# Kernel optimization log

Hardware: AMD Instinct MI355X
Metric: run time of the kernel (lower is better)

Reference implementation:

```python
import jax, jax.numpy as jnp
import numpy as np

N_NODES = 100000
N_EDGES = 1250000
N_GRAPHS = 1024
NUM_SHAPES = 16
NUM_COLORS = 16
NUM_CLASSES = 10


def setup_inputs() -> dict:
    key = jax.random.key(0)
    ks = jax.random.split(key, 16)
    x_tokens = jax.random.randint(ks[0], (N_NODES, 2), 0, NUM_SHAPES, dtype=jnp.int64) if jax.config.jax_enable_x64 else jax.random.randint(ks[0], (N_NODES, 2), 0, NUM_SHAPES, dtype=jnp.int32)
    edge_index = jax.random.randint(ks[1], (2, N_EDGES), 0, N_NODES, dtype=jnp.int32)
    batch = jnp.sort(jax.random.randint(ks[2], (N_NODES,), 0, N_GRAPHS, dtype=jnp.int32))
    def glorot(k, shape, fan_in):
        return jax.random.normal(k, shape, jnp.float32) / jnp.sqrt(jnp.float32(fan_in))
    return {
        "x_tokens": x_tokens,
        "edge_index": edge_index,
        "batch": batch,
        "shape_emb": jax.random.normal(ks[3], (NUM_SHAPES, 8), jnp.float32),
        "color_emb": jax.random.normal(ks[4], (NUM_COLORS, 8), jnp.float32),
        "lin_w": glorot(ks[5], (32, 16), 16),
        "lin_b": jnp.zeros((32,), jnp.float32),
        "conv1_wrel": glorot(ks[6], (64, 32), 32),
        "conv1_brel": jnp.zeros((64,), jnp.float32),
        "conv1_wroot": glorot(ks[7], (64, 32), 32),
        "conv2_wrel": glorot(ks[8], (64, 64), 64),
        "conv2_brel": jnp.zeros((64,), jnp.float32),
        "conv2_wroot": glorot(ks[9], (64, 64), 64),
        "cls_w": glorot(ks[10], (NUM_CLASSES, 64), 64),
        "cls_b": jnp.zeros((NUM_CLASSES,), jnp.float32),
    }


def _graph_conv(x, src, dst, w_rel, b_rel, w_root):
    # PyG GraphConv (aggr='add'): out_i = W_rel @ sum_{j->i} x_j + b_rel + W_root @ x_i
    agg = jax.ops.segment_sum(x[src], dst, num_segments=x.shape[0])  # [N, d_in]
    return agg @ w_rel.T + b_rel + x @ w_root.T


def reference(x_tokens, edge_index, batch, shape_emb, color_emb, lin_w, lin_b,
              conv1_wrel, conv1_brel, conv1_wroot,
              conv2_wrel, conv2_brel, conv2_wroot, cls_w, cls_b):
    src, dst = edge_index[0], edge_index[1]
    # embed shape/color tokens and concat -> [N, 16]
    x = jnp.concatenate([shape_emb[x_tokens[:, 0]], color_emb[x_tokens[:, 1]]], axis=1)
    x = jax.nn.relu(x @ lin_w.T + lin_b)                      # [N, 32]
    x = jax.nn.relu(_graph_conv(x, src, dst, conv1_wrel, conv1_brel, conv1_wroot))  # [N, 64]
    x = jax.nn.relu(_graph_conv(x, src, dst, conv2_wrel, conv2_brel, conv2_wroot))  # [N, 64]
    # global mean pool over graphs
    sums = jax.ops.segment_sum(x, batch, num_segments=N_GRAPHS)           # [G, 64]
    counts = jax.ops.segment_sum(jnp.ones((x.shape[0],), x.dtype), batch, num_segments=N_GRAPHS)
    pooled = sums / jnp.maximum(counts, 1.0)[:, None]
    return pooled @ cls_w.T + cls_b                            # [G, num_classes]
```

## Files before the change

kernel.cpp:

```cpp
#include <hip/hip_runtime.h>

#define N_NODES  100000
#define N_EDGES  1250000
#define N_GRAPHS 1024
#define NB       ((N_NODES + 127) >> 7)
#define NB2      (N_NODES / 16)
#define NBLK_F   500
#define EPB      (N_EDGES / NBLK_F)
#define EMB_BLKS ((N_NODES + 255) / 256)
#define CAP      512

typedef __attribute__((ext_vector_type(8))) short short8;
typedef __attribute__((ext_vector_type(4))) float f32x4;
union U16 { uint4 u; short8 s; };

__device__ __forceinline__ float bflo(unsigned int w) { return __uint_as_float(w << 16); }
__device__ __forceinline__ float bfhi(unsigned int w) { return __uint_as_float(w & 0xffff0000u); }
__device__ __forceinline__ unsigned short f2bf(float f) {
  unsigned int u = __float_as_uint(f);
  u = (u + 0x7fffu + ((u >> 16) & 1u)) >> 16;
  return (unsigned short)u;
}
__device__ __forceinline__ unsigned int pack2(float a, float b) {
  return (unsigned int)f2bf(a) | ((unsigned int)f2bf(b) << 16);
}

template <int DIN>
__device__ __forceinline__ void prep_body(int t, const float* __restrict__ wrel,
                                          const float* __restrict__ wroot,
                                          unsigned short* __restrict__ Bf) {
  constexpr int NKC = (2 * DIN) / 32;
  if (t >= NKC * 4 * 64) return;
  int l = t & 63;
  int ct = (t >> 6) & 3;
  int kc = t >> 8;
  int col = ct * 16 + (l & 15);
#pragma unroll
  for (int e = 0; e < 8; ++e) {
    int k = kc * 32 + ((l >> 4) << 3) + e;
    float v = (k < DIN) ? wrel[col * DIN + k] : wroot[col * DIN + (k - DIN)];
    Bf[(size_t)t * 8 + e] = f2bf(v);
  }
}

__global__ void __launch_bounds__(256)
k_front(const int* __restrict__ tok,
        const float* __restrict__ semb, const float* __restrict__ cemb,
        const float* __restrict__ lw, const float* __restrict__ lb,
        unsigned short* __restrict__ x1,
        const float* __restrict__ w1rel, const float* __restrict__ w1root,
        const float* __restrict__ w2rel, const float* __restrict__ w2root,
        unsigned short* __restrict__ Bf1, unsigned short* __restrict__ Bf2,
        const int* __restrict__ dst, int* __restrict__ hist) {
  __shared__ int lh[NB];
  const int t = threadIdx.x;
  const int bid = blockIdx.x;
  if (bid < EMB_BLKS) {
    int i = bid * 256 + t;
    if (i >= N_NODES) return;
    int s = tok[2 * i], c = tok[2 * i + 1];
    float e[16];
#pragma unroll
    for (int k = 0; k < 8; ++k) { e[k] = semb[s * 8 + k]; e[8 + k] = cemb[c * 8 + k]; }
    unsigned int w[16];
#pragma unroll
    for (int o = 0; o < 16; ++o) {
      float a0 = lb[2 * o], a1 = lb[2 * o + 1];
#pragma unroll
      for (int k = 0; k < 16; ++k) {
        a0 = fmaf(e[k], lw[(2 * o) * 16 + k], a0);
        a1 = fmaf(e[k], lw[(2 * o + 1) * 16 + k], a1);
      }
      w[o] = pack2(fmaxf(a0, 0.f), fmaxf(a1, 0.f));
    }
    uint4* d4 = (uint4*)(x1 + (size_t)i * 32);
#pragma unroll
    for (int q = 0; q < 4; ++q)
      d4[q] = make_uint4(w[4 * q], w[4 * q + 1], w[4 * q + 2], w[4 * q + 3]);
  } else if (bid < EMB_BLKS + 6) {
    int pb = bid - EMB_BLKS;
    if (pb < 2) prep_body<32>(pb * 256 + t, w1rel, w1root, Bf1);
    else prep_body<64>((pb - 2) * 256 + t, w2rel, w2root, Bf2);
  } else {
    const int blk = bid - EMB_BLKS - 6;
    for (int i = t; i < NB; i += 256) lh[i] = 0;
    __syncthreads();
    const int start = blk * EPB;
    for (int e = start + t; e < start + EPB; e += 256)
      atomicAdd(&lh[dst[e] >> 7], 1);
    __syncthreads();
    int* hrow = hist + (size_t)blk * NB;
    for (int i = t; i < NB; i += 256)
      hrow[i] = lh[i];
  }
}

__global__ void __launch_bounds__(512)
k_colscan(int* __restrict__ hist, int* __restrict__ btotal) {
  __shared__ int sc[512];
  const int b = blockIdx.x;
  const int t = threadIdx.x;
  int v = (t < NBLK_F) ? hist[(size_t)t * NB + b] : 0;
  sc[t] = v;
  __syncthreads();
  for (int off = 1; off < 512; off <<= 1) {
    int x = (t >= off) ? sc[t - off] : 0;
    __syncthreads();
    sc[t] += x;
    __syncthreads();
  }
  if (t < NBLK_F) hist[(size_t)t * NB + b] = sc[t] - v;
  if (t == 511) btotal[b] = sc[511];
}

__global__ void __launch_bounds__(1024)
k_bscan(const int* __restrict__ btotal, int* __restrict__ bbase) {
  __shared__ int s[1024];
  int t = threadIdx.x;
  int d = (t < NB) ? btotal[t] : 0;
  s[t] = d;
  __syncthreads();
  for (int off = 1; off < 1024; off <<= 1) {
    int v = (t >= off) ? s[t - off] : 0;
    __syncthreads();
    s[t] += v;
    __syncthreads();
  }
  if (t < NB) bbase[t] = s[t] - d;
}

__global__ void __launch_bounds__(256)
k_bfill(const int* __restrict__ src, const int* __restrict__ dst,
        const int* __restrict__ bbase, const int* __restrict__ hist,
        int* __restrict__ tmp) {
  __shared__ int cur[NB];
  const int t = threadIdx.x;
  const int blk = blockIdx.x;
  const int* hrow = hist + (size_t)blk * NB;
  for (int i = t; i < NB; i += 256)
    cur[i] = bbase[i] + hrow[i];
  __syncthreads();
  const int start = blk * EPB;
  for (int e = start + t; e < start + EPB; e += 256) {
    int d = dst[e];
    int pos = atomicAdd(&cur[d >> 7], 1);
    tmp[pos] = (src[e] << 7) | (d & 127);
  }
}

__global__ void __launch_bounds__(256)
k_bfinal(const int* __restrict__ bbase, const int* __restrict__ btotal,
         const int* __restrict__ tmp,
         int* __restrict__ deg, int* __restrict__ rowst,
         int* __restrict__ esrc) {
  __shared__ int h[128], sc[128], cur[128];
  const int t = threadIdx.x;
  const int b = blockIdx.x;
  const int base = bbase[b], cnt = btotal[b];
  if (t < 128) h[t] = 0;
  __syncthreads();
  for (int i = t; i < cnt; i += 256) atomicAdd(&h[tmp[base + i] & 127], 1);
  __syncthreads();
  if (t < 128) sc[t] = h[t];
  __syncthreads();
  for (int off = 1; off < 128; off <<= 1) {
    int v = 0;
    if (t < 128 && t >= off) v = sc[t - off];
    __syncthreads();
    if (t < 128) sc[t] += v;
    __syncthreads();
  }
  if (t < 128) {
    int excl = sc[t] - h[t];
    cur[t] = excl;
    int node = (b << 7) + t;
    if (node < N_NODES) { deg[node] = h[t]; rowst[node] = base + excl; }
  }
  __syncthreads();
  for (int i = t; i < cnt; i += 256) {
    int v = tmp[base + i];
    int p = atomicAdd(&cur[v & 127], 1);
    esrc[base + p] = v >> 7;
  }
}

template <int DIN>
__global__ void __launch_bounds__(256)
k_conv(const int* __restrict__ deg, const int* __restrict__ rowst,
       const int* __restrict__ esrc,
       const unsigned short* __restrict__ X,
       const uint4* __restrict__ Bf,
       const float* __restrict__ bias,
       unsigned short* __restrict__ Y) {
  constexpr int NKC = (2 * DIN) / 32;
  constexpr int LPGu = DIN / 4;
  constexpr int GROUPS = 64 / LPGu;
  __shared__ int lsrc[CAP];
  __shared__ int hdeg[16], hbase[16];
  __shared__ int s_cnt, s_base;
  __shared__ unsigned short aggT[(DIN / 8) * 16 * 8];
  const int t = threadIdx.x;
  const int lane = t & 63;
  const int wv = t >> 6;
  const int b = blockIdx.x;
  if (t < 16) hdeg[t] = deg[b * 16 + t];
  __syncthreads();
  if (t == 0) {
    int run = 0;
#pragma unroll
    for (int n = 0; n < 16; ++n) { hbase[n] = run; run += hdeg[n]; }
    s_cnt = min(run, CAP);
    s_base = rowst[b * 16];
  }
  __syncthreads();
  const int cnt = s_cnt, base = s_base;
  for (int i = t; i < cnt; i += 256) lsrc[i] = esrc[base + i];
  __syncthreads();

  const int sub = lane / LPGu;
  const int lg = lane % LPGu;
#pragma unroll
  for (int k = 0; k < 4; ++k) {
    const int n = wv * 4 + k;
    const int dgn = hdeg[n];
    const int eb = hbase[n];
    float a0 = 0.f, a1 = 0.f, a2 = 0.f, a3 = 0.f;
    for (int j = 0; j < dgn; j += 2 * GROUPS) {
      int e0 = j + sub, e1 = j + GROUPS + sub;
      int s0 = lsrc[min(eb + min(e0, dgn - 1), CAP - 1)];
      int s1 = lsrc[min(eb + min(e1, dgn - 1), CAP - 1)];
      uint2 r0 = *((const uint2*)(X + (size_t)s0 * DIN) + lg);
      uint2 r1 = *((const uint2*)(X + (size_t)s1 * DIN) + lg);
      if (e0 < dgn) { a0 += bflo(r0.x); a1 += bfhi(r0.x); a2 += bflo(r0.y); a3 += bfhi(r0.y); }
      if (e1 < dgn) { a0 += bflo(r1.x); a1 += bfhi(r1.x); a2 += bflo(r1.y); a3 += bfhi(r1.y); }
    }
#pragma unroll
    for (int off = LPGu; off < 64; off <<= 1) {
      a0 += __shfl_xor(a0, off);
      a1 += __shfl_xor(a1, off);
      a2 += __shfl_xor(a2, off);
      a3 += __shfl_xor(a3, off);
    }
    if (sub == 0) {
      uint2 w; w.x = pack2(a0, a1); w.y = pack2(a2, a3);
      *(uint2*)&aggT[(((lg >> 1) * 16 + n) << 3) + ((lg & 1) << 2)] = w;
    }
  }
  __syncthreads();

  short8 bf[NKC];
#pragma unroll
  for (int kc = 0; kc < NKC; ++kc) { U16 u; u.u = Bf[(kc * 4 + wv) * 64 + lane]; bf[kc] = u.s; }
  const float bc = bias[wv * 16 + (lane & 15)];
  const int r = lane & 15;
  const int gg = b * 16 + r;
  short8 a[NKC];
#pragma unroll
  for (int kc = 0; kc < NKC / 2; ++kc) {
    const int chunk = kc * 4 + (lane >> 4);
    U16 u; u.u = *(const uint4*)&aggT[(chunk * 16 + r) << 3];
    a[kc] = u.s;
  }
#pragma unroll
  for (int kc = NKC / 2; kc < NKC; ++kc) {
    const int colx = (kc - NKC / 2) * 32 + ((lane >> 4) << 3);
    U16 u; u.u = *(const uint4*)(X + (size_t)gg * DIN + colx);
    a[kc] = u.s;
  }
  f32x4 acc = {bc, bc, bc, bc};
#pragma unroll
  for (int kc = 0; kc < NKC; ++kc)
    acc = __builtin_amdgcn_mfma_f32_16x16x32_bf16(a[kc], bf[kc], acc, 0, 0, 0);
  const int col = wv * 16 + (lane & 15);
#pragma unroll
  for (int j = 0; j < 4; ++j) {
    int grow = b * 16 + ((lane >> 4) << 2) + j;
    Y[(size_t)grow * 64 + col] = f2bf(fmaxf(acc[j], 0.f));
  }
}

__global__ void __launch_bounds__(256)
k_pool(const unsigned short* __restrict__ y2,
       const int* __restrict__ batch,
       const float* __restrict__ cw, const float* __restrict__ cb,
       float* __restrict__ out) {
  __shared__ float part[4][64];
  const int g = blockIdx.x;
  const int lane = threadIdx.x & 63;
  const int wv = threadIdx.x >> 6;
  int lo = 0, hi = N_NODES;
  while (lo < hi) { int m = (lo + hi) >> 1; if (batch[m] < g) lo = m + 1; else hi = m; }
  int lo2 = lo, hi2 = N_NODES;
  while (lo2 < hi2) { int m = (lo2 + hi2) >> 1; if (batch[m] < g + 1) lo2 = m + 1; else hi2 = m; }
  float s = 0.f;
  for (int r = lo + wv; r < lo2; r += 4)
    s += __uint_as_float((unsigned int)y2[(size_t)r * 64 + lane] << 16);
  part[wv][lane] = s;
  __syncthreads();
  if (wv == 0) {
    float p = part[0][lane] + part[1][lane] + part[2][lane] + part[3][lane];
    int c_ = lo2 - lo;
    p *= 1.f / (float)(c_ > 0 ? c_ : 1);
    for (int c = 0; c < 10; ++c) {
      float v = p * cw[c * 64 + lane];
#pragma unroll
      for (int off = 1; off < 64; off <<= 1) v += __shfl_xor(v, off);
      if (lane == 0) out[g * 10 + c] = v + cb[c];
    }
  }
}

extern "C" void kernel_launch(void* const* d_in, const int* in_sizes, int n_in,
                              void* d_out, int out_size, void* d_ws, size_t ws_size,
                              hipStream_t stream) {
  const int*   tok    = (const int*)d_in[0];
  const int*   eidx   = (const int*)d_in[1];
  const int*   batch  = (const int*)d_in[2];
  const float* semb   = (const float*)d_in[3];
  const float* cemb   = (const float*)d_in[4];
  const float* lw     = (const float*)d_in[5];
  const float* lb     = (const float*)d_in[6];
  const float* w1rel  = (const float*)d_in[7];
  const float* b1     = (const float*)d_in[8];
  const float* w1root = (const float*)d_in[9];
  const float* w2rel  = (const float*)d_in[10];
  const float* b2     = (const float*)d_in[11];
  const float* w2root = (const float*)d_in[12];
  const float* cw     = (const float*)d_in[13];
  const float* cb     = (const float*)d_in[14];
  const int* src = eidx;
  const int* dst = eidx + N_EDGES;

  char* p = (char*)d_ws;
  unsigned short* X1 = (unsigned short*)p;  p += (size_t)N_NODES * 32 * 2;
  unsigned short* X2 = (unsigned short*)p;  p += (size_t)N_NODES * 64 * 2;
  unsigned short* Y2 = (unsigned short*)p;  p += (size_t)N_NODES * 64 * 2;
  int*   tmp    = (int*)p;  p += (size_t)N_EDGES * 4;
  int*   esrc   = (int*)p;  p += (size_t)N_EDGES * 4;
  int*   degv   = (int*)p;  p += (size_t)N_NODES * 4;
  int*   rowst  = (int*)p;  p += (size_t)N_NODES * 4;
  int*   hist   = (int*)p;  p += (size_t)NBLK_F * NB * 4;
  int*   btotal = (int*)p;  p += 4096;
  int*   bbase  = (int*)p;  p += 4096;
  unsigned short* Bf1 = (unsigned short*)p;  p += 512 * 8 * 2;
  unsigned short* Bf2 = (unsigned short*)p;  p += 1024 * 8 * 2;

  k_front<<<EMB_BLKS + 6 + NBLK_F, 256, 0, stream>>>(
      tok, semb, cemb, lw, lb, X1,
      w1rel, w1root, w2rel, w2root, Bf1, Bf2, dst, hist);

  k_colscan<<<NB, 512, 0, stream>>>(hist, btotal);
  k_bscan<<<1, 1024, 0, stream>>>(btotal, bbase);
  k_bfill<<<NBLK_F, 256, 0, stream>>>(src, dst, bbase, hist, tmp);
  k_bfinal<<<NB, 256, 0, stream>>>(bbase, btotal, tmp, degv, rowst, esrc);

  k_conv<32><<<NB2, 256, 0, stream>>>(degv, rowst, esrc, X1, (const uint4*)Bf1, b1, X2);
  k_conv<64><<<NB2, 256, 0, stream>>>(degv, rowst, esrc, X2, (const uint4*)Bf2, b2, Y2);

  k_pool<<<N_GRAPHS, 256, 0, stream>>>(Y2, batch, cw, cb, (float*)d_out);
}
```

Measured before the change: 135.4 us.

## Fold bucket-base scan into fill/final kernels and widen conv gathers to 16B

Drops the single-block k_bscan launch. Each k_bfill block now recomputes the exclusive scan of btotal redundantly, and each k_bfinal block computes its base by reducing the preceding btotal entries, which removes one launch and its serialization gap. The conv aggregation also switches from 8-byte to 16-byte row loads per lane, so fewer lanes cover each row and more edges are processed in parallel per wave. The cost is redundant scan work in every block and more accumulator registers.

New measurement: 151.9 us. +12.1%, slower.

```diff
diff --git a/kernel.cpp b/kernel.cpp
--- a/kernel.cpp
+++ b/kernel.cpp
@@ -113,32 +113,37 @@
   if (t == 511) btotal[b] = sc[511];
 }
 
-__global__ void __launch_bounds__(1024)
-k_bscan(const int* __restrict__ btotal, int* __restrict__ bbase) {
-  __shared__ int s[1024];
-  int t = threadIdx.x;
-  int d = (t < NB) ? btotal[t] : 0;
-  s[t] = d;
-  __syncthreads();
-  for (int off = 1; off < 1024; off <<= 1) {
-    int v = (t >= off) ? s[t - off] : 0;
-    __syncthreads();
-    s[t] += v;
-    __syncthreads();
-  }
-  if (t < NB) bbase[t] = s[t] - d;
-}
-
 __global__ void __launch_bounds__(256)
 k_bfill(const int* __restrict__ src, const int* __restrict__ dst,
-        const int* __restrict__ bbase, const int* __restrict__ hist,
+        const int* __restrict__ btotal, const int* __restrict__ hist,
         int* __restrict__ tmp) {
   __shared__ int cur[NB];
+  __shared__ int spart[256];
   const int t = threadIdx.x;
   const int blk = blockIdx.x;
   const int* hrow = hist + (size_t)blk * NB;
-  for (int i = t; i < NB; i += 256)
-    cur[i] = bbase[i] + hrow[i];
+  int v[4]; int s = 0;
+#pragma unroll
+  for (int j = 0; j < 4; ++j) {
+    int idx = t * 4 + j;
+    v[j] = (idx < NB) ? btotal[idx] : 0;
+    s += v[j];
+  }
+  spart[t] = s;
+  __syncthreads();
+  for (int off = 1; off < 256; off <<= 1) {
+    int x = (t >= off) ? spart[t - off] : 0;
+    __syncthreads();
+    spart[t] += x;
+    __syncthreads();
+  }
+  int run = spart[t] - s;
+#pragma unroll
+  for (int j = 0; j < 4; ++j) {
+    int idx = t * 4 + j;
+    if (idx < NB) cur[idx] = run + hrow[idx];
+    run += v[j];
+  }
   __syncthreads();
   const int start = blk * EPB;
   for (int e = start + t; e < start + EPB; e += 256) {
@@ -149,16 +154,26 @@
 }
 
 __global__ void __launch_bounds__(256)
-k_bfinal(const int* __restrict__ bbase, const int* __restrict__ btotal,
-         const int* __restrict__ tmp,
+k_bfinal(const int* __restrict__ btotal, const int* __restrict__ tmp,
          int* __restrict__ deg, int* __restrict__ rowst,
          int* __restrict__ esrc) {
+  __shared__ int spart[256];
   __shared__ int h[128], sc[128], cur[128];
+  __shared__ int s_base;
   const int t = threadIdx.x;
   const int b = blockIdx.x;
-  const int base = bbase[b], cnt = btotal[b];
+  int s = 0;
+  for (int i = t; i < b; i += 256) s += btotal[i];
+  spart[t] = s;
   if (t < 128) h[t] = 0;
   __syncthreads();
+  for (int off = 128; off >= 1; off >>= 1) {
+    if (t < off) spart[t] += spart[t + off];
+    __syncthreads();
+  }
+  if (t == 0) s_base = spart[0];
+  __syncthreads();
+  const int base = s_base, cnt = btotal[b];
   for (int i = t; i < cnt; i += 256) atomicAdd(&h[tmp[base + i] & 127], 1);
   __syncthreads();
   if (t < 128) sc[t] = h[t];
@@ -193,8 +208,8 @@
        const float* __restrict__ bias,
        unsigned short* __restrict__ Y) {
   constexpr int NKC = (2 * DIN) / 32;
-  constexpr int LPGu = DIN / 4;
-  constexpr int GROUPS = 64 / LPGu;
+  constexpr int LPG = DIN / 8;
+  constexpr int GROUPS = 64 / LPG;
   __shared__ int lsrc[CAP];
   __shared__ int hdeg[16], hbase[16];
   __shared__ int s_cnt, s_base;
@@ -217,33 +232,42 @@
   for (int i = t; i < cnt; i += 256) lsrc[i] = esrc[base + i];
   __syncthreads();
 
-  const int sub = lane / LPGu;
-  const int lg = lane % LPGu;
+  const int sub = lane / LPG;
+  const int lg = lane % LPG;
 #pragma unroll
   for (int k = 0; k < 4; ++k) {
     const int n = wv * 4 + k;
     const int dgn = hdeg[n];
     const int eb = hbase[n];
     float a0 = 0.f, a1 = 0.f, a2 = 0.f, a3 = 0.f;
+    float a4 = 0.f, a5 = 0.f, a6 = 0.f, a7 = 0.f;
     for (int j = 0; j < dgn; j += 2 * GROUPS) {
       int e0 = j + sub, e1 = j + GROUPS + sub;
       int s0 = lsrc[min(eb + min(e0, dgn - 1), CAP - 1)];
       int s1 = lsrc[min(eb + min(e1, dgn - 1), CAP - 1)];
-      uint2 r0 = *((const uint2*)(X + (size_t)s0 * DIN) + lg);
-      uint2 r1 = *((const uint2*)(X + (size_t)s1 * DIN) + lg);
-      if (e0 < dgn) { a0 += bflo(r0.x); a1 += bfhi(r0.x); a2 += bflo(r0.y); a3 += bfhi(r0.y); }
-      if (e1 < dgn) { a0 += bflo(r1.x); a1 += bfhi(r1.x); a2 += bflo(r1.y); a3 += bfhi(r1.y); }
-    }
-#pragma unroll
-    for (int off = LPGu; off < 64; off <<= 1) {
-      a0 += __shfl_xor(a0, off);
-      a1 += __shfl_xor(a1, off);
-      a2 += __shfl_xor(a2, off);
-      a3 += __shfl_xor(a3, off);
+      uint4 r0 = *((const uint4*)(X + (size_t)s0 * DIN) + lg);
+      uint4 r1 = *((const uint4*)(X + (size_t)s1 * DIN) + lg);
+      if (e0 < dgn) {
+        a0 += bflo(r0.x); a1 += bfhi(r0.x); a2 += bflo(r0.y); a3 += bfhi(r0.y);
+        a4 += bflo(r0.z); a5 += bfhi(r0.z); a6 += bflo(r0.w); a7 += bfhi(r0.w);
+      }
+      if (e1 < dgn) {
+        a0 += bflo(r1.x); a1 += bfhi(r1.x); a2 += bflo(r1.y); a3 += bfhi(r1.y);
+        a4 += bflo(r1.z); a5 += bfhi(r1.z); a6 += bflo(r1.w); a7 += bfhi(r1.w);
+      }
+    }
+#pragma unroll
+    for (int off = LPG; off < 64; off <<= 1) {
+      a0 += __shfl_xor(a0, off); a1 += __shfl_xor(a1, off);
+      a2 += __shfl_xor(a2, off); a3 += __shfl_xor(a3, off);
+      a4 += __shfl_xor(a4, off); a5 += __shfl_xor(a5, off);
+      a6 += __shfl_xor(a6, off); a7 += __shfl_xor(a7, off);
     }
     if (sub == 0) {
-      uint2 w; w.x = pack2(a0, a1); w.y = pack2(a2, a3);
-      *(uint2*)&aggT[(((lg >> 1) * 16 + n) << 3) + ((lg & 1) << 2)] = w;
+      uint4 w;
+      w.x = pack2(a0, a1); w.y = pack2(a2, a3);
+      w.z = pack2(a4, a5); w.w = pack2(a6, a7);
+      *(uint4*)&aggT[(lg * 16 + n) << 3] = w;
     }
   }
   __syncthreads();
@@ -341,7 +365,6 @@
   int*   rowst  = (int*)p;  p += (size_t)N_NODES * 4;
   int*   hist   = (int*)p;  p += (size_t)NBLK_F * NB * 4;
   int*   btotal = (int*)p;  p += 4096;
-  int*   bbase  = (int*)p;  p += 4096;
   unsigned short* Bf1 = (unsigned short*)p;  p += 512 * 8 * 2;
   unsigned short* Bf2 = (unsigned short*)p;  p += 1024 * 8 * 2;
 
@@ -350,9 +373,8 @@
       w1rel, w1root, w2rel, w2root, Bf1, Bf2, dst, hist);
 
   k_colscan<<<NB, 512, 0, stream>>>(hist, btotal);
-  k_bscan<<<1, 1024, 0, stream>>>(btotal, bbase);
-  k_bfill<<<NBLK_F, 256, 0, stream>>>(src, dst, bbase, hist, tmp);
-  k_bfinal<<<NB, 256, 0, stream>>>(bbase, btotal, tmp, degv, rowst, esrc);
+  k_bfill<<<NBLK_F, 256, 0, stream>>>(src, dst, btotal, hist, tmp);
+  k_bfinal<<<NB, 256, 0, stream>>>(btotal, tmp, degv, rowst, esrc);
 
   k_conv<32><<<NB2, 256, 0, stream>>>(degv, rowst, esrc, X1, (const uint4*)Bf1, b1, X2);
   k_conv<64><<<NB2, 256, 0, stream>>>(degv, rowst, esrc, X2, (const uint4*)Bf2, b2, Y2);
```
